# Optimization experiments

Measured on AMD Instinct MI355X. Metric: run time of the kernel, lower is better.

The kernel has to match this reference:

```python
import jax, jax.numpy as jnp
import numpy as np

B, L, H, NL = 4, 384, 128, 3
F = H * NL  # num_filters = hidden_dim * num_layers = h_V feature dim


def gelu(x):
    return jax.nn.gelu(x, approximate=False)  # torch nn.GELU default is exact erf


def setup_inputs() -> dict:
    key = jax.random.key(0)
    ks = jax.random.split(key, 10)
    rn = lambda k, shape, s=0.05: jax.random.normal(k, shape, jnp.float32) * s
    h_V = jax.random.normal(ks[0], (B, L, F), jnp.float32)
    h_E = jax.random.normal(ks[1], (B, L, L, H), jnp.float32)
    mask = (jax.random.uniform(ks[2], (B, L)) > 0.1).astype(jnp.float32)
    # CFConv filter_network: Linear(H->F), GELU, Linear(F->F), GELU
    fw1 = rn(ks[3], (H, F)); fb1 = jnp.zeros((F,), jnp.float32)
    fw2 = rn(ks[4], (F, F)); fb2 = jnp.zeros((F,), jnp.float32)
    # mlp_head: Linear(F->H), GELU, Linear(H->H//2), GELU, Linear(H//2->1)
    hw1 = rn(ks[5], (F, H)); hb1 = jnp.zeros((H,), jnp.float32)
    hw2 = rn(ks[6], (H, H // 2)); hb2 = jnp.zeros((H // 2,), jnp.float32)
    hw3 = rn(ks[7], (H // 2, 1)); hb3 = jnp.zeros((1,), jnp.float32)
    return dict(h_V=h_V, h_E=h_E, mask=mask, fw1=fw1, fb1=fb1, fw2=fw2, fb2=fb2,
                hw1=hw1, hb1=hb1, hw2=hw2, hb2=hb2, hw3=hw3, hb3=hb3)


def reference(h_V, h_E, mask, fw1, fb1, fw2, fb2, hw1, hb1, hw2, hb2, hw3, hb3):
    # CFConv: per-edge filter MLP on edge features [B,L,L,H] -> [B,L,L,F]
    Wf = gelu(gelu(h_E @ fw1 + fb1) @ fw2 + fb2)
    # broadcast multiply with x.unsqueeze(1) then sum over neighbor dim (dim=2)
    x_conv = jnp.einsum('bkf,blkf->blf', h_V, Wf)  # [B,L,F]
    # mlp_head (dropout is identity in eval)
    h = gelu(x_conv @ hw1 + hb1)
    h = gelu(h @ hw2 + hb2)
    pred = (h @ hw3 + hb3)[..., 0]  # [B,L]
    valid_length = jnp.clip(jnp.sum(mask, axis=1), 1.0, None)
    return jnp.sum(pred * mask, axis=1) / jnp.sqrt(valid_length)  # [B]
```

## Files before the change

### kernel.cpp

```cpp
#include <hip/hip_runtime.h>
#include <hip/hip_bf16.h>


#define Bz 4
#define Lz 384
#define Hz 128
#define Fz 384
#define KT 64
#define NIT 6

typedef short bf16x8 __attribute__((ext_vector_type(8)));
typedef float f32x4 __attribute__((ext_vector_type(4)));

__device__ __forceinline__ unsigned short f2bf(float f) {
  unsigned int u = __float_as_uint(f);
  u += 0x7FFFu + ((u >> 16) & 1u);
  return (unsigned short)(u >> 16);
}

__device__ __forceinline__ float gelu_f(float x) {
  const float a1 = 0.254829592f, a2 = -0.284496736f, a3 = 1.421413741f;
  const float a4 = -1.453152027f, a5 = 1.061405429f;
  float z = fabsf(x) * 0.7071067811865476f;
  float t = __builtin_amdgcn_rcpf(__builtin_fmaf(0.3275911f, z, 1.0f));
  float poly = t * (a1 + t * (a2 + t * (a3 + t * (a4 + t * a5))));
  float e = __builtin_fmaf(-poly, __expf(-z * z), 1.0f);
  return 0.5f * x * (1.0f + copysignf(e, x));
}

__global__ __launch_bounds__(256) void prep_kernel(
    const float* __restrict__ fw1, const float* __restrict__ fw2,
    unsigned short* __restrict__ fw1P, unsigned short* __restrict__ fw2P,
    float* __restrict__ accbuf, int* __restrict__ ctr)
{
  int e = blockIdx.x * 256 + threadIdx.x;
  if (e < 16) accbuf[e] = 0.0f;
  if (e == 16) *ctr = 0;
  if (e < 24 * 4 * 64 * 8) {
    int j = e & 7, lf = (e >> 3) & 63, ks = (e >> 9) & 3, t = e >> 11;
    int n = t * 16 + (lf & 15);
    int k = ks * 32 + (lf >> 4) * 8 + j;
    fw1P[e] = f2bf(fw1[(size_t)k * Fz + n]);
  } else if (e < 24 * 4 * 64 * 8 + 24 * 12 * 64 * 8) {
    int o = e - 24 * 4 * 64 * 8;
    int j = o & 7, lf = (o >> 3) & 63, r = o >> 9;
    int ks = r % 12, t = r / 12;
    int n = t * 16 + (lf & 15);
    int k = ks * 32 + (lf >> 4) * 8 + j;
    fw2P[o] = f2bf(fw2[(size_t)k * Fz + n]);
  }
}

__global__ __launch_bounds__(512, 4) void schnet_main(
    const float* __restrict__ hV, const float* __restrict__ hE,
    const float* __restrict__ mask,
    const unsigned short* __restrict__ fw1P, const float* __restrict__ fb1,
    const unsigned short* __restrict__ fw2P, const float* __restrict__ fb2,
    const float* __restrict__ hw1, const float* __restrict__ hb1,
    const float* __restrict__ hw2, const float* __restrict__ hb2,
    const float* __restrict__ hw3, const float* __restrict__ hb3,
    float* __restrict__ accbuf, int* __restrict__ ctr,
    float* __restrict__ out)
{
  const int bl   = blockIdx.x;
  const int b    = bl / Lz;
  const int l    = bl - b * Lz;
  const int tid  = threadIdx.x;
  const int wave = tid >> 6;
  const int lane = tid & 63;
  const int lr   = lane & 15;
  const int quad = lane >> 4;

  __shared__ unsigned short sT1[KT][392];
  __shared__ unsigned short sA[KT][136];
  __shared__ float sXC[Fz];
  __shared__ float sHp[4][Hz];
  __shared__ float sH1[Hz];
  __shared__ float sH2[64];
  __shared__ int   sLast;

  float* sStage = (float*)&sT1[0][0];

  const float* hE_bl = hE + (size_t)bl * (Lz * Hz);
  const unsigned short* w1base = fw1P + (size_t)lane * 8;
  const unsigned short* w2base = fw2P + (size_t)lane * 8;

  const f32x4 zero4 = {0.f, 0.f, 0.f, 0.f};
  f32x4 xc[3];
  xc[0] = zero4; xc[1] = zero4; xc[2] = zero4;

  for (int it = 0; it < NIT; ++it) {
    __syncthreads();

    {
      const char* gt = (const char*)(hE_bl + (size_t)it * (KT * Hz));
      #pragma unroll
      for (int j = 0; j < 4; ++j) {
        int chunk = (j * 8 + wave) * 1024;
        __builtin_amdgcn_global_load_lds(
            (const __attribute__((address_space(1))) void*)(gt + chunk + lane * 16),
            (__attribute__((address_space(3))) void*)((char*)sStage + chunk),
            16, 0, 0);
      }
    }
    __syncthreads();

    #pragma unroll
    for (int s = 0; s < 4; ++s) {
      int f = 4 * tid + 2048 * s;
      float4 v = *(const float4*)(sStage + f);
      int row = f >> 7, col = f & 127;
      short4 o;
      o.x = (short)f2bf(v.x); o.y = (short)f2bf(v.y);
      o.z = (short)f2bf(v.z); o.w = (short)f2bf(v.w);
      *(short4*)&sA[row][col] = o;
    }
    __syncthreads();

    {
      f32x4 acc[4][3];
      #pragma unroll
      for (int mt = 0; mt < 4; ++mt)
        #pragma unroll
        for (int nt = 0; nt < 3; ++nt) acc[mt][nt] = zero4;

      #pragma unroll 2
      for (int ks = 0; ks < 4; ++ks) {
        const int k0 = ks * 32 + quad * 8;
        bf16x8 afr[4];
        #pragma unroll
        for (int mt = 0; mt < 4; ++mt)
          afr[mt] = *(const bf16x8*)(&sA[mt * 16 + lr][k0]);
        bf16x8 bfr[3];
        #pragma unroll
        for (int nt = 0; nt < 3; ++nt)
          bfr[nt] = *(const bf16x8*)(w1base +
                        (size_t)(((wave * 3 + nt) * 4 + ks) * 64) * 8);
        #pragma unroll
        for (int mt = 0; mt < 4; ++mt)
          #pragma unroll
          for (int nt = 0; nt < 3; ++nt)
            acc[mt][nt] = __builtin_amdgcn_mfma_f32_16x16x32_bf16(
                bfr[nt], afr[mt], acc[mt][nt], 0, 0, 0);
      }
      #pragma unroll
      for (int nt = 0; nt < 3; ++nt) {
        const int n0 = wave * 48 + nt * 16 + quad * 4;
        const f32x4 bias = *(const f32x4*)(fb1 + n0);
        #pragma unroll
        for (int mt = 0; mt < 4; ++mt) {
          short4 o;
          o.x = (short)f2bf(gelu_f(acc[mt][nt][0] + bias[0]));
          o.y = (short)f2bf(gelu_f(acc[mt][nt][1] + bias[1]));
          o.z = (short)f2bf(gelu_f(acc[mt][nt][2] + bias[2]));
          o.w = (short)f2bf(gelu_f(acc[mt][nt][3] + bias[3]));
          *(short4*)&sT1[mt * 16 + lr][n0] = o;
        }
      }
    }
    __syncthreads();

    {
      f32x4 acc[4][3];
      #pragma unroll
      for (int mt = 0; mt < 4; ++mt)
        #pragma unroll
        for (int nt = 0; nt < 3; ++nt) acc[mt][nt] = zero4;

      #pragma unroll 2
      for (int ks = 0; ks < 12; ++ks) {
        const int k0 = ks * 32 + quad * 8;
        bf16x8 afr[4];
        #pragma unroll
        for (int mt = 0; mt < 4; ++mt)
          afr[mt] = *(const bf16x8*)(&sT1[mt * 16 + lr][k0]);
        bf16x8 bfr[3];
        #pragma unroll
        for (int nt = 0; nt < 3; ++nt)
          bfr[nt] = *(const bf16x8*)(w2base +
                        (size_t)(((wave * 3 + nt) * 12 + ks) * 64) * 8);
        #pragma unroll
        for (int mt = 0; mt < 4; ++mt)
          #pragma unroll
          for (int nt = 0; nt < 3; ++nt)
            acc[mt][nt] = __builtin_amdgcn_mfma_f32_16x16x32_bf16(
                bfr[nt], afr[mt], acc[mt][nt], 0, 0, 0);
      }
      #pragma unroll
      for (int nt = 0; nt < 3; ++nt) {
        const int n0 = wave * 48 + nt * 16 + quad * 4;
        const f32x4 b2 = *(const f32x4*)(fb2 + n0);
        #pragma unroll
        for (int mt = 0; mt < 4; ++mt) {
          const float* hv =
              hV + ((size_t)b * Lz + it * KT + mt * 16 + lr) * Fz + n0;
          const f32x4 hvv = *(const f32x4*)hv;
          #pragma unroll
          for (int r = 0; r < 4; ++r)
            xc[nt][r] += gelu_f(acc[mt][nt][r] + b2[r]) * hvv[r];
        }
      }
    }
  }

  #pragma unroll
  for (int nt = 0; nt < 3; ++nt)
    #pragma unroll
    for (int r = 0; r < 4; ++r) {
      float v = xc[nt][r];
      v += __shfl_xor(v, 1);
      v += __shfl_xor(v, 2);
      v += __shfl_xor(v, 4);
      v += __shfl_xor(v, 8);
      if (lr == 0) sXC[wave * 48 + nt * 16 + quad * 4 + r] = v;
    }
  __syncthreads();

  {
    int i = tid & 127;
    int part = tid >> 7;
    float a = 0.f;
    const int f0 = part * 96;
    for (int f = f0; f < f0 + 96; ++f) a += sXC[f] * hw1[f * Hz + i];
    sHp[part][i] = a;
  }
  __syncthreads();
  if (tid < Hz)
    sH1[tid] = gelu_f(sHp[0][tid] + sHp[1][tid] + sHp[2][tid] + sHp[3][tid]
                      + hb1[tid]);
  __syncthreads();
  if (tid < 64) {
    float a = hb2[tid];
    for (int i = 0; i < Hz; ++i) a += sH1[i] * hw2[i * 64 + tid];
    sH2[tid] = gelu_f(a);
  }
  __syncthreads();
  if (wave == 0) {
    float v = sH2[lane] * hw3[lane];
    #pragma unroll
    for (int off = 32; off >= 1; off >>= 1) v += __shfl_xor(v, off);
    if (lane == 0) {
      float pred = v + hb3[0];
      atomicAdd(&accbuf[b], pred * mask[b * Lz + l]);
      __threadfence();
      sLast = (atomicAdd(ctr, 1) == (Bz * Lz - 1));
    }
  }
  __syncthreads();

  if (sLast && wave < Bz) {
    float s = 0.f;
    #pragma unroll
    for (int k = 0; k < Lz / 64; ++k) s += mask[wave * Lz + k * 64 + lane];
    #pragma unroll
    for (int off = 32; off >= 1; off >>= 1) s += __shfl_xor(s, off);
    if (lane == 0) {
      float vl = s < 1.0f ? 1.0f : s;
      float a = atomicAdd(&accbuf[wave], 0.0f);
      out[wave] = a / sqrtf(vl);
    }
  }
}

extern "C" void kernel_launch(void* const* d_in, const int* in_sizes, int n_in,
                              void* d_out, int out_size, void* d_ws, size_t ws_size,
                              hipStream_t stream)
{
  const float* hV   = (const float*)d_in[0];
  const float* hE   = (const float*)d_in[1];
  const float* mask = (const float*)d_in[2];
  const float* fw1  = (const float*)d_in[3];
  const float* fb1  = (const float*)d_in[4];
  const float* fw2  = (const float*)d_in[5];
  const float* fb2  = (const float*)d_in[6];
  const float* hw1  = (const float*)d_in[7];
  const float* hb1  = (const float*)d_in[8];
  const float* hw2  = (const float*)d_in[9];
  const float* hb2  = (const float*)d_in[10];
  const float* hw3  = (const float*)d_in[11];
  const float* hb3  = (const float*)d_in[12];
  float* out = (float*)d_out;

  float* accbuf = (float*)d_ws;
  int*   ctr    = (int*)((char*)d_ws + 64);
  unsigned short* fw1P = (unsigned short*)((char*)d_ws + 1024);
  unsigned short* fw2P = fw1P + 24 * 4 * 64 * 8;

  prep_kernel<<<768, 256, 0, stream>>>(fw1, fw2, fw1P, fw2P, accbuf, ctr);
  schnet_main<<<Bz * Lz, 512, 0, stream>>>(hV, hE, mask, fw1P, fb1, fw2P, fb2,
                                           hw1, hb1, hw2, hb2, hw3, hb3,
                                           accbuf, ctr, out);
}
```

Measured before the change: 872.1 us.

## Pre-convert h_E to swizzled bf16 in prep and prefetch next tile during GEMM2

The prep kernel now converts the whole h_E tensor to bf16 in an XOR-swizzled layout, so the main kernel loads bf16 tiles straight into LDS with no in-kernel conversion pass or staging buffer. The next tile's load is issued after GEMM1 and overlaps GEMM2, which removes two barriers per iteration. The sA and sT1 LDS layouts are swizzled to cut bank conflicts, and s_setprio wraps the MFMA blocks. In exchange there is an extra full read and write of h_E in the prep kernel, plus a workspace buffer of about 150 MB.

```diff
diff --git a/kernel.cpp b/kernel.cpp
--- a/kernel.cpp
+++ b/kernel.cpp
@@ -1,5 +1,4 @@
 #include <hip/hip_runtime.h>
-#include <hip/hip_bf16.h>
 
 
 #define Bz 4
@@ -8,6 +7,7 @@
 #define Fz 384
 #define KT 64
 #define NIT 6
+#define TILE_B (KT * Hz * 2)
 
 typedef short bf16x8 __attribute__((ext_vector_type(8)));
 typedef float f32x4 __attribute__((ext_vector_type(4)));
@@ -30,7 +30,9 @@
 
 __global__ __launch_bounds__(256) void prep_kernel(
     const float* __restrict__ fw1, const float* __restrict__ fw2,
+    const float* __restrict__ hE,
     unsigned short* __restrict__ fw1P, unsigned short* __restrict__ fw2P,
+    unsigned short* __restrict__ hEP,
     float* __restrict__ accbuf, int* __restrict__ ctr)
 {
   int e = blockIdx.x * 256 + threadIdx.x;
@@ -49,10 +51,27 @@
     int k = ks * 32 + (lf >> 4) * 8 + j;
     fw2P[o] = f2bf(fw2[(size_t)k * Fz + n]);
   }
+  if (e < Bz * Lz * NIT * KT * 16) {
+    int u = e & 15;
+    int r = (e >> 4) & 63;
+    int tile = e >> 10;
+    int it = tile % NIT;
+    int bl = tile / NIT;
+    const float* src = hE + (size_t)bl * (Lz * Hz)
+                       + (size_t)(it * KT + r) * Hz + ((u ^ (r & 7)) << 3);
+    f32x4 v0 = *(const f32x4*)src;
+    f32x4 v1 = *(const f32x4*)(src + 4);
+    bf16x8 o;
+    o[0] = (short)f2bf(v0[0]); o[1] = (short)f2bf(v0[1]);
+    o[2] = (short)f2bf(v0[2]); o[3] = (short)f2bf(v0[3]);
+    o[4] = (short)f2bf(v1[0]); o[5] = (short)f2bf(v1[1]);
+    o[6] = (short)f2bf(v1[2]); o[7] = (short)f2bf(v1[3]);
+    *(bf16x8*)(hEP + (size_t)e * 8) = o;
+  }
 }
 
 __global__ __launch_bounds__(512, 4) void schnet_main(
-    const float* __restrict__ hV, const float* __restrict__ hE,
+    const float* __restrict__ hV, const unsigned short* __restrict__ hEP,
     const float* __restrict__ mask,
     const unsigned short* __restrict__ fw1P, const float* __restrict__ fb1,
     const unsigned short* __restrict__ fw2P, const float* __restrict__ fb2,
@@ -70,18 +89,18 @@
   const int lane = tid & 63;
   const int lr   = lane & 15;
   const int quad = lane >> 4;
-
-  __shared__ unsigned short sT1[KT][392];
-  __shared__ unsigned short sA[KT][136];
-  __shared__ float sXC[Fz];
-  __shared__ float sHp[4][Hz];
-  __shared__ float sH1[Hz];
-  __shared__ float sH2[64];
-  __shared__ int   sLast;
-
-  float* sStage = (float*)&sT1[0][0];
-
-  const float* hE_bl = hE + (size_t)bl * (Lz * Hz);
+  const int l7   = lane & 7;
+
+  __shared__ __attribute__((aligned(16))) char sMem[65536];
+  unsigned short* sA  = (unsigned short*)sMem;
+  unsigned short* sT1 = (unsigned short*)(sMem + 16384);
+  float* sXC = (float*)sMem;
+  float* sHp = sXC + Fz;
+  float* sH1 = sHp + 4 * Hz;
+  float* sH2 = sH1 + Hz;
+  int*   sLast = (int*)(sH2 + 64);
+
+  const char* hEPt = (const char*)hEP + (size_t)bl * (NIT * TILE_B);
   const unsigned short* w1base = fw1P + (size_t)lane * 8;
   const unsigned short* w2base = fw2P + (size_t)lane * 8;
 
@@ -89,34 +108,16 @@
   f32x4 xc[3];
   xc[0] = zero4; xc[1] = zero4; xc[2] = zero4;
 
+  #pragma unroll
+  for (int j = 0; j < 2; ++j) {
+    int off = (j * 8 + wave) << 10;
+    __builtin_amdgcn_global_load_lds(
+        (const __attribute__((address_space(1))) void*)(hEPt + off + lane * 16),
+        (__attribute__((address_space(3))) void*)(sMem + off), 16, 0, 0);
+  }
+  __syncthreads();
+
   for (int it = 0; it < NIT; ++it) {
-    __syncthreads();
-
-    {
-      const char* gt = (const char*)(hE_bl + (size_t)it * (KT * Hz));
-      #pragma unroll
-      for (int j = 0; j < 4; ++j) {
-        int chunk = (j * 8 + wave) * 1024;
-        __builtin_amdgcn_global_load_lds(
-            (const __attribute__((address_space(1))) void*)(gt + chunk + lane * 16),
-            (__attribute__((address_space(3))) void*)((char*)sStage + chunk),
-            16, 0, 0);
-      }
-    }
-    __syncthreads();
-
-    #pragma unroll
-    for (int s = 0; s < 4; ++s) {
-      int f = 4 * tid + 2048 * s;
-      float4 v = *(const float4*)(sStage + f);
-      int row = f >> 7, col = f & 127;
-      short4 o;
-      o.x = (short)f2bf(v.x); o.y = (short)f2bf(v.y);
-      o.z = (short)f2bf(v.z); o.w = (short)f2bf(v.w);
-      *(short4*)&sA[row][col] = o;
-    }
-    __syncthreads();
-
     {
       f32x4 acc[4][3];
       #pragma unroll
@@ -126,27 +127,31 @@
 
       #pragma unroll 2
       for (int ks = 0; ks < 4; ++ks) {
-        const int k0 = ks * 32 + quad * 8;
+        const int xu = ((ks << 2) + quad) ^ l7;
         bf16x8 afr[4];
         #pragma unroll
         for (int mt = 0; mt < 4; ++mt)
-          afr[mt] = *(const bf16x8*)(&sA[mt * 16 + lr][k0]);
+          afr[mt] = *(const bf16x8*)(sA + ((mt * 16 + lr) << 7) + (xu << 3));
         bf16x8 bfr[3];
         #pragma unroll
         for (int nt = 0; nt < 3; ++nt)
           bfr[nt] = *(const bf16x8*)(w1base +
                         (size_t)(((wave * 3 + nt) * 4 + ks) * 64) * 8);
+        __builtin_amdgcn_s_setprio(1);
         #pragma unroll
         for (int mt = 0; mt < 4; ++mt)
           #pragma unroll
           for (int nt = 0; nt < 3; ++nt)
             acc[mt][nt] = __builtin_amdgcn_mfma_f32_16x16x32_bf16(
                 bfr[nt], afr[mt], acc[mt][nt], 0, 0, 0);
+        __builtin_amdgcn_s_setprio(0);
       }
       #pragma unroll
       for (int nt = 0; nt < 3; ++nt) {
         const int n0 = wave * 48 + nt * 16 + quad * 4;
         const f32x4 bias = *(const f32x4*)(fb1 + n0);
+        const int so = (((wave * 6 + nt * 2 + (quad >> 1)) ^ l7) << 3)
+                       + ((quad & 1) << 2);
         #pragma unroll
         for (int mt = 0; mt < 4; ++mt) {
           short4 o;
@@ -154,11 +159,22 @@
           o.y = (short)f2bf(gelu_f(acc[mt][nt][1] + bias[1]));
           o.z = (short)f2bf(gelu_f(acc[mt][nt][2] + bias[2]));
           o.w = (short)f2bf(gelu_f(acc[mt][nt][3] + bias[3]));
-          *(short4*)&sT1[mt * 16 + lr][n0] = o;
+          *(short4*)(sT1 + (mt * 16 + lr) * 384 + so) = o;
         }
       }
     }
     __syncthreads();
+
+    if (it + 1 < NIT) {
+      const char* gt = hEPt + (it + 1) * TILE_B;
+      #pragma unroll
+      for (int j = 0; j < 2; ++j) {
+        int off = (j * 8 + wave) << 10;
+        __builtin_amdgcn_global_load_lds(
+            (const __attribute__((address_space(1))) void*)(gt + off + lane * 16),
+            (__attribute__((address_space(3))) void*)(sMem + off), 16, 0, 0);
+      }
+    }
 
     {
       f32x4 acc[4][3];
@@ -169,22 +185,24 @@
 
       #pragma unroll 2
       for (int ks = 0; ks < 12; ++ks) {
-        const int k0 = ks * 32 + quad * 8;
+        const int xu = ((ks << 2) + quad) ^ l7;
         bf16x8 afr[4];
         #pragma unroll
         for (int mt = 0; mt < 4; ++mt)
-          afr[mt] = *(const bf16x8*)(&sT1[mt * 16 + lr][k0]);
+          afr[mt] = *(const bf16x8*)(sT1 + (mt * 16 + lr) * 384 + (xu << 3));
         bf16x8 bfr[3];
         #pragma unroll
         for (int nt = 0; nt < 3; ++nt)
           bfr[nt] = *(const bf16x8*)(w2base +
                         (size_t)(((wave * 3 + nt) * 12 + ks) * 64) * 8);
+        __builtin_amdgcn_s_setprio(1);
         #pragma unroll
         for (int mt = 0; mt < 4; ++mt)
           #pragma unroll
           for (int nt = 0; nt < 3; ++nt)
             acc[mt][nt] = __builtin_amdgcn_mfma_f32_16x16x32_bf16(
                 bfr[nt], afr[mt], acc[mt][nt], 0, 0, 0);
+        __builtin_amdgcn_s_setprio(0);
       }
       #pragma unroll
       for (int nt = 0; nt < 3; ++nt) {
@@ -201,6 +219,7 @@
         }
       }
     }
+    __syncthreads();
   }
 
   #pragma unroll
@@ -222,12 +241,12 @@
     float a = 0.f;
     const int f0 = part * 96;
     for (int f = f0; f < f0 + 96; ++f) a += sXC[f] * hw1[f * Hz + i];
-    sHp[part][i] = a;
+    sHp[part * Hz + i] = a;
   }
   __syncthreads();
   if (tid < Hz)
-    sH1[tid] = gelu_f(sHp[0][tid] + sHp[1][tid] + sHp[2][tid] + sHp[3][tid]
-                      + hb1[tid]);
+    sH1[tid] = gelu_f(sHp[tid] + sHp[Hz + tid] + sHp[2 * Hz + tid]
+                      + sHp[3 * Hz + tid] + hb1[tid]);
   __syncthreads();
   if (tid < 64) {
     float a = hb2[tid];
@@ -243,12 +262,12 @@
       float pred = v + hb3[0];
       atomicAdd(&accbuf[b], pred * mask[b * Lz + l]);
       __threadfence();
-      sLast = (atomicAdd(ctr, 1) == (Bz * Lz - 1));
-    }
-  }
-  __syncthreads();
-
-  if (sLast && wave < Bz) {
+      *sLast = (atomicAdd(ctr, 1) == (Bz * Lz - 1));
+    }
+  }
+  __syncthreads();
+
+  if (*sLast && wave < Bz) {
     float s = 0.f;
     #pragma unroll
     for (int k = 0; k < Lz / 64; ++k) s += mask[wave * Lz + k * 64 + lane];
@@ -285,9 +304,12 @@
   int*   ctr    = (int*)((char*)d_ws + 64);
   unsigned short* fw1P = (unsigned short*)((char*)d_ws + 1024);
   unsigned short* fw2P = fw1P + 24 * 4 * 64 * 8;
-
-  prep_kernel<<<768, 256, 0, stream>>>(fw1, fw2, fw1P, fw2P, accbuf, ctr);
-  schnet_main<<<Bz * Lz, 512, 0, stream>>>(hV, hE, mask, fw1P, fb1, fw2P, fb2,
+  unsigned short* hEP  = fw2P + 24 * 12 * 64 * 8;
+
+  const int units = Bz * Lz * NIT * KT * 16;
+  prep_kernel<<<units / 256, 256, 0, stream>>>(fw1, fw2, hE, fw1P, fw2P, hEP,
+                                               accbuf, ctr);
+  schnet_main<<<Bz * Lz, 512, 0, stream>>>(hV, hEP, mask, fw1P, fb1, fw2P, fb2,
                                            hw1, hb1, hw2, hb2, hw3, hb3,
                                            accbuf, ctr, out);
 }
```

After: 875.6 us. No clear change (+0.4%).
